# Optimization experiments

Hardware: AMD Instinct MI355X
Metric: run time of the kernel (lower is better)

The kernel has to match this reference:

```python
import jax, jax.numpy as jnp
import numpy as np
import math

D = 1024
FFN = 4096
NHEADS = 8
HEAD_DIM = D // NHEADS
RL_DIM = 4
LN_EPS = 1e-5


def _layer_norm(x, gamma, beta):
    mu = jnp.mean(x, axis=-1, keepdims=True)
    var = jnp.var(x, axis=-1, keepdims=True)
    return (x - mu) * jax.lax.rsqrt(var + LN_EPS) * gamma + beta


def setup_inputs() -> dict:
    key = jax.random.key(0)
    ks = jax.random.split(key, 12)
    B, L = 2, 2048
    s = 1.0 / math.sqrt(D)
    inp = {
        "h": jax.random.normal(ks[0], (B, L, D), dtype=jnp.float32),
        "rh": jax.random.normal(ks[1], (B, L, RL_DIM), dtype=jnp.float32),
        "Wq": jax.random.normal(ks[2], (D, D), dtype=jnp.float32) * s,
        "Wk": jax.random.normal(ks[3], (D, D), dtype=jnp.float32) * s,
        "Wv": jax.random.normal(ks[4], (D, D), dtype=jnp.float32) * s,
        "Wo": jax.random.normal(ks[5], (D, D), dtype=jnp.float32) * s,
        "Wrk": jax.random.normal(ks[6], (RL_DIM, RL_DIM), dtype=jnp.float32) * 0.5,
        "Wrq": jax.random.normal(ks[7], (RL_DIM, RL_DIM), dtype=jnp.float32) * 0.5,
        "W1": jax.random.normal(ks[8], (D, FFN), dtype=jnp.float32) * s,
        "b1": jnp.zeros((FFN,), dtype=jnp.float32),
        "W2": jax.random.normal(ks[9], (FFN, D), dtype=jnp.float32) / math.sqrt(FFN),
        "b2": jnp.zeros((D,), dtype=jnp.float32),
        "g1": jnp.ones((D,), dtype=jnp.float32),
        "be1": jnp.zeros((D,), dtype=jnp.float32),
        "g2": jnp.ones((D,), dtype=jnp.float32),
        "be2": jnp.zeros((D,), dtype=jnp.float32),
    }
    return inp


def reference(h, rh, Wq, Wk, Wv, Wo, Wrk, Wrq, W1, b1, W2, b2, g1, be1, g2, be2):
    B, L, _ = h.shape
    q = h @ Wq  # [B, L, D]
    k = h @ Wk
    v = h @ Wv
    # Faithful to the torch code: .view() reshapes (NOT transposes).
    q_ = q.reshape(B, NHEADS, L, HEAD_DIM)
    k_ = k.reshape(B, NHEADS, L, HEAD_DIM)
    v_ = v.reshape(B, NHEADS, L, HEAD_DIM)
    k_t = k_.reshape(B, NHEADS, HEAD_DIM, L)  # reshape, not transpose, as in source
    score = jnp.einsum("bnld,bndm->bnlm", q_, k_t) / math.sqrt(HEAD_DIM)
    # relative-position bias (rl=True path)
    r_k = rh @ Wrk  # [B, L, rl_dim]
    r_q = rh @ Wrq
    r_q_ = r_q[:, None]  # [B, 1, L, rl_dim]
    r_k_t = r_k[:, None].reshape(B, 1, RL_DIM, L)  # reshape, as in source
    score = score + jnp.einsum("bnlr,bnrm->bnlm", r_q_, r_k_t) / 2.0
    attn = jax.nn.softmax(score, axis=-1)
    context = jnp.einsum("bnlm,bnmd->bnld", attn, v_)
    h_sa = context.reshape(B, L, D) @ Wo
    h1 = _layer_norm(h_sa + h, g1, be1)
    hf = jax.nn.relu(h1 @ W1 + b1) @ W2 + b2
    h2 = _layer_norm(h1 + hf, g2, be2)
    return h2
```

## Files before the change

kernel.cpp:

```cpp
#include <hip/hip_runtime.h>

typedef __bf16 bf16;
typedef __bf16 bf16x8 __attribute__((ext_vector_type(8)));
typedef __bf16 bf16x4 __attribute__((ext_vector_type(4)));
typedef float  f32x4  __attribute__((ext_vector_type(4)));

#define D_     1024
#define FFN_   4096
#define NH_    8
#define HD_    128
#define L_     2048
#define B_     2
#define ROWS_  4096
#define PAIRS_ 16
#define KT_    64
#define PSTR   72
#define ALPHA_  0.08838834764831845f
#define RSCALE_ 5.656854249492381f

__device__ __forceinline__ void async16(const bf16* g, bf16* l) {
    __builtin_amdgcn_global_load_lds(
        (const __attribute__((address_space(1))) unsigned int*)g,
        (__attribute__((address_space(3))) unsigned int*)l, 16, 0, 0);
}
__device__ __forceinline__ f32x4 MFMA(bf16x8 a, bf16x8 b, f32x4 c) {
    return __builtin_amdgcn_mfma_f32_16x16x32_bf16(a, b, c, 0, 0, 0);
}

__global__ void cvt_bf16_kernel(const float* __restrict__ in, bf16* __restrict__ out) {
    long i = ((long)blockIdx.x * 256 + threadIdx.x) * 4;
    float4 v = *(const float4*)(in + i);
    bf16x4 o = {(bf16)v.x, (bf16)v.y, (bf16)v.z, (bf16)v.w};
    *(bf16x4*)(out + i) = o;
}

template<typename TI>
__global__ void transpose_to_bf16(const TI* __restrict__ in, bf16* __restrict__ out,
                                  int r, int c, long sIn, long sOut) {
    __shared__ bf16 t[32][33];
    long zi = (long)blockIdx.z * sIn;
    long zo = (long)blockIdx.z * sOut;
    int x0 = blockIdx.x * 32, y0 = blockIdx.y * 32;
    int tx = threadIdx.x & 31, ty = threadIdx.x >> 5;
#pragma unroll
    for (int i = 0; i < 4; i++)
        t[ty + i * 8][tx] = (bf16)in[zi + (long)(y0 + ty + i * 8) * c + x0 + tx];
    __syncthreads();
#pragma unroll
    for (int i = 0; i < 4; i++)
        out[zo + (long)(x0 + ty + i * 8) * r + y0 + tx] = t[tx][ty + i * 8];
}

__global__ void rqk_kernel(const float* __restrict__ rh, const float* __restrict__ Wrq,
                           const float* __restrict__ Wrk, float* __restrict__ rq,
                           float* __restrict__ rk) {
    int t = blockIdx.x * 256 + threadIdx.x;
    float4 r = *(const float4*)(rh + (long)t * 4);
    float q[4], k[4];
#pragma unroll
    for (int c = 0; c < 4; c++) {
        q[c] = r.x * Wrq[c] + r.y * Wrq[4 + c] + r.z * Wrq[8 + c] + r.w * Wrq[12 + c];
        k[c] = r.x * Wrk[c] + r.y * Wrk[4 + c] + r.z * Wrk[8 + c] + r.w * Wrk[12 + c];
    }
    float4 qo = {q[0], q[1], q[2], q[3]};
    float4 ko = {k[0], k[1], k[2], k[3]};
    *(float4*)(rq + (long)t * 4) = qo;
    *(float4*)(rk + (long)t * 4) = ko;
}

template<int BM, int EPI>
__launch_bounds__(256)
__global__ void gemm128(const bf16* __restrict__ A, const bf16* __restrict__ Bt,
                        void* __restrict__ Cv, const float* __restrict__ bias,
                        int M, int N, int K, int lda, int ldb,
                        long sA, long sB, long sC, float alpha) {
    constexpr int RF = (BM == 128) ? 4 : 2;
    __shared__ __align__(16) bf16 As[BM * 32];
    __shared__ __align__(16) bf16 Bs[128 * 32];
    const int tid  = threadIdx.x;
    const int wave = tid >> 6, lane = tid & 63;
    const int quad = lane >> 4, mr = lane & 15;
    const int bM = blockIdx.x * BM, bN = blockIdx.y * 128;
    A  += (long)blockIdx.z * sA;
    Bt += (long)blockIdx.z * sB;
    const int wr = (wave >> 1) * (BM / 2), wc = (wave & 1) * 64;

    f32x4 acc[RF][4];
#pragma unroll
    for (int r = 0; r < RF; r++)
#pragma unroll
        for (int c = 0; c < 4; c++) { f32x4 z = {0.f, 0.f, 0.f, 0.f}; acc[r][c] = z; }

    const int scol = (lane & 3) * 8;
    const bf16* Ag0; const bf16* Ag1 = nullptr;
    if (BM == 128) {
        const int srow = wave * 32 + (lane >> 2);
        Ag0 = A + (long)(bM + srow) * lda + scol;
        Ag1 = Ag0 + (long)16 * lda;
    } else {
        const int srow = wave * 16 + (lane >> 2);
        Ag0 = A + (long)(bM + srow) * lda + scol;
    }
    const int srowB = wave * 32 + (lane >> 2);
    const bf16* Bg0 = Bt + (long)(bN + srowB) * ldb + scol;
    const bf16* Bg1 = Bg0 + (long)16 * ldb;
    bf16* AsW = As + wave * (BM == 128 ? 1024 : 512);
    bf16* BsW = Bs + wave * 1024;

    for (int k0 = 0; k0 < K; k0 += 32) {
        if (BM == 128) { async16(Ag0, AsW); async16(Ag1, AsW + 512); Ag0 += 32; Ag1 += 32; }
        else           { async16(Ag0, AsW); Ag0 += 32; }
        async16(Bg0, BsW); async16(Bg1, BsW + 512);
        Bg0 += 32; Bg1 += 32;
        __syncthreads();
        bf16x8 af[RF], bfv[4];
#pragma unroll
        for (int r = 0; r < RF; r++)
            af[r] = *(const bf16x8*)(&As[(wr + r * 16 + mr) * 32 + quad * 8]);
#pragma unroll
        for (int c = 0; c < 4; c++)
            bfv[c] = *(const bf16x8*)(&Bs[(wc + c * 16 + mr) * 32 + quad * 8]);
#pragma unroll
        for (int r = 0; r < RF; r++)
#pragma unroll
            for (int c = 0; c < 4; c++)
                acc[r][c] = MFMA(af[r], bfv[c], acc[r][c]);
        __syncthreads();
    }

    const long zC = (long)blockIdx.z * sC;
    float bias_c[4];
    if (EPI & 1) {
#pragma unroll
        for (int c = 0; c < 4; c++) bias_c[c] = bias[bN + wc + c * 16 + mr];
    }
#pragma unroll
    for (int r = 0; r < RF; r++) {
#pragma unroll
        for (int c = 0; c < 4; c++) {
            const long col = bN + wc + c * 16 + mr;
#pragma unroll
            for (int i = 0; i < 4; i++) {
                const long row = bM + wr + r * 16 + quad * 4 + i;
                float v = acc[r][c][i] * alpha;
                if (EPI & 1) v += bias_c[c];
                if (EPI & 2) v = fmaxf(v, 0.f);
                if (EPI & 4) ((bf16*)Cv)[zC + row * (long)N + col] = (bf16)v;
                else         ((float*)Cv)[zC + row * (long)N + col] = v;
            }
        }
    }
}

__launch_bounds__(256, 1)
__global__ void flash_attn(const bf16* __restrict__ qb, const bf16* __restrict__ kT,
                           const bf16* __restrict__ vT, const float* __restrict__ rq,
                           const float* __restrict__ rk, bf16* __restrict__ ctx) {
    __shared__ __align__(16) bf16  Ks[2][KT_ * HD_];
    __shared__ __align__(16) bf16  Vs[2][HD_ * KT_];
    __shared__ __align__(16) float rks[2][4 * KT_];
    __shared__ __align__(16) bf16  Ps[4][32 * PSTR];

    const int tid = threadIdx.x, wave = tid >> 6, lane = tid & 63;
    const int quad = lane >> 4, mr = lane & 15;
    const int pair = blockIdx.y, b = pair >> 3;
    const int bQ = blockIdx.x * 128;
    const long PB = (long)pair * L_ * HD_;
    const bf16* Qg = qb + PB;
    const bf16* Kg = kT + PB;
    const bf16* Vg = vT + PB;
    const float* rkb = rk + (long)b * L_ * 4;

    bf16x8 Qf[2][4], Qe[2];
#pragma unroll
    for (int f = 0; f < 2; f++) {
#pragma unroll
        for (int t = 0; t < 4; t++)
            Qf[f][t] = *(const bf16x8*)(Qg + (long)(bQ + wave * 32 + f * 16 + mr) * HD_ + t * 32 + quad * 8);
        bf16x8 z = {};
        if (quad == 0) {
            float4 v = *(const float4*)(rq + ((long)b * L_ + bQ + wave * 32 + f * 16 + mr) * 4);
            z[0] = (bf16)(v.x * RSCALE_); z[1] = (bf16)(v.y * RSCALE_);
            z[2] = (bf16)(v.z * RSCALE_); z[3] = (bf16)(v.w * RSCALE_);
        }
        Qe[f] = z;
    }

    bf16x8 ones;
#pragma unroll
    for (int j = 0; j < 8; j++) ones[j] = (bf16)1.0f;

    f32x4 O[2][8], Osum[2];
#pragma unroll
    for (int f = 0; f < 2; f++) {
#pragma unroll
        for (int c = 0; c < 8; c++) { f32x4 z = {0.f, 0.f, 0.f, 0.f}; O[f][c] = z; }
        f32x4 z = {0.f, 0.f, 0.f, 0.f}; Osum[f] = z;
    }

#define STAGE_TILES(buf, kt0)                                                              \
    {                                                                                      \
        _Pragma("unroll")                                                                  \
        for (int it = 0; it < 4; it++) {                                                   \
            int G = it * 256 + tid;                                                        \
            int r1 = G >> 4, g1 = (G & 15) ^ (r1 & 15);                                    \
            async16(Kg + (long)((kt0) + r1) * HD_ + g1 * 8, &Ks[buf][(it * 256 + wave * 64) * 8]); \
            int r2 = G >> 3, g2 = (G & 7) ^ (r2 & 7);                                      \
            async16(Vg + (long)r2 * L_ + (kt0) + g2 * 8, &Vs[buf][(it * 256 + wave * 64) * 8]);    \
        }                                                                                  \
        if (tid < 64) {                                                                    \
            int r3 = tid >> 4, g3 = tid & 15;                                              \
            async16((const bf16*)(rkb + (long)r3 * L_ + (kt0) + g3 * 4), (bf16*)&rks[buf][0]); \
        }                                                                                  \
    }

    STAGE_TILES(0, 0)
    __syncthreads();

    for (int kt = 0; kt < L_ / KT_; kt++) {
        const int cur = kt & 1;
        if (kt + 1 < L_ / KT_) STAGE_TILES(cur ^ 1, (kt + 1) * KT_)

        const bf16* KsB = Ks[cur];
        const bf16* VsB = Vs[cur];
        const float* rksB = rks[cur];
        bf16* PsW = Ps[wave];

        f32x4 sc[4][2];
#pragma unroll
        for (int c = 0; c < 4; c++) {
            f32x4 s0 = {0.f, 0.f, 0.f, 0.f}, s1 = s0;
#pragma unroll
            for (int t = 0; t < 4; t++) {
                bf16x8 kf = *(const bf16x8*)(KsB + (c * 16 + mr) * HD_ + (((t * 4 + quad) ^ mr) * 8));
                s0 = MFMA(Qf[0][t], kf, s0);
                s1 = MFMA(Qf[1][t], kf, s1);
            }
            bf16x8 ke = {};
            if (quad == 0) {
                ke[0] = (bf16)rksB[0 * KT_ + c * 16 + mr];
                ke[1] = (bf16)rksB[1 * KT_ + c * 16 + mr];
                ke[2] = (bf16)rksB[2 * KT_ + c * 16 + mr];
                ke[3] = (bf16)rksB[3 * KT_ + c * 16 + mr];
            }
            s0 = MFMA(Qe[0], ke, s0);
            s1 = MFMA(Qe[1], ke, s1);
            sc[c][0] = s0; sc[c][1] = s1;
        }

#pragma unroll
        for (int f = 0; f < 2; f++) {
#pragma unroll
            for (int i = 0; i < 4; i++) {
                const int prow = (f * 16 + quad * 4 + i) * PSTR;
                PsW[prow + 0 * 16 + mr] = (bf16)__expf(sc[0][f][i] * ALPHA_);
                PsW[prow + 1 * 16 + mr] = (bf16)__expf(sc[1][f][i] * ALPHA_);
                PsW[prow + 2 * 16 + mr] = (bf16)__expf(sc[2][f][i] * ALPHA_);
                PsW[prow + 3 * 16 + mr] = (bf16)__expf(sc[3][f][i] * ALPHA_);
            }
        }

#pragma unroll
        for (int t = 0; t < 2; t++) {
            bf16x8 pf0 = *(const bf16x8*)(PsW + (0 * 16 + mr) * PSTR + t * 32 + quad * 8);
            bf16x8 pf1 = *(const bf16x8*)(PsW + (1 * 16 + mr) * PSTR + t * 32 + quad * 8);
            Osum[0] = MFMA(pf0, ones, Osum[0]);
            Osum[1] = MFMA(pf1, ones, Osum[1]);
#pragma unroll
            for (int c2 = 0; c2 < 8; c2++) {
                bf16x8 vf = *(const bf16x8*)(VsB + (c2 * 16 + mr) * KT_ + (((t * 4 + quad) ^ (mr & 7)) * 8));
                O[0][c2] = MFMA(pf0, vf, O[0][c2]);
                O[1][c2] = MFMA(pf1, vf, O[1][c2]);
            }
        }
        __syncthreads();
    }

    bf16* Cg = ctx + PB;
#pragma unroll
    for (int f = 0; f < 2; f++)
#pragma unroll
        for (int i = 0; i < 4; i++) {
            const float inv = 1.f / Osum[f][i];
            const long row = bQ + wave * 32 + f * 16 + quad * 4 + i;
#pragma unroll
            for (int c2 = 0; c2 < 8; c2++)
                Cg[row * HD_ + c2 * 16 + mr] = (bf16)(O[f][c2][i] * inv);
        }
#undef STAGE_TILES
}

__global__ void layernorm_res(const float* __restrict__ x1, const float* __restrict__ x2,
                              const float* __restrict__ g, const float* __restrict__ be,
                              float* __restrict__ outf, bf16* __restrict__ outb) {
    const int row = blockIdx.x, tid = threadIdx.x;
    const long base = (long)row * D_ + tid * 4;
    float4 a = *(const float4*)(x1 + base);
    float4 b = *(const float4*)(x2 + base);
    float x[4] = {a.x + b.x, a.y + b.y, a.z + b.z, a.w + b.w};
    float s = x[0] + x[1] + x[2] + x[3];
    float s2 = x[0] * x[0] + x[1] * x[1] + x[2] * x[2] + x[3] * x[3];
#pragma unroll
    for (int off = 32; off; off >>= 1) { s += __shfl_xor(s, off, 64); s2 += __shfl_xor(s2, off, 64); }
    __shared__ float ps[4], ps2[4];
    int wave = tid >> 6, lane = tid & 63;
    if (lane == 0) { ps[wave] = s; ps2[wave] = s2; }
    __syncthreads();
    s  = ps[0] + ps[1] + ps[2] + ps[3];
    s2 = ps2[0] + ps2[1] + ps2[2] + ps2[3];
    float mean = s * (1.f / D_);
    float var  = s2 * (1.f / D_) - mean * mean;
    float rstd = rsqrtf(var + 1e-5f);
    float4 gg = *(const float4*)(g + tid * 4);
    float4 bb = *(const float4*)(be + tid * 4);
    float y0 = (x[0] - mean) * rstd * gg.x + bb.x;
    float y1 = (x[1] - mean) * rstd * gg.y + bb.y;
    float y2 = (x[2] - mean) * rstd * gg.z + bb.z;
    float y3 = (x[3] - mean) * rstd * gg.w + bb.w;
    float4 yo = {y0, y1, y2, y3};
    *(float4*)(outf + base) = yo;
    bf16x4 ob = {(bf16)y0, (bf16)y1, (bf16)y2, (bf16)y3};
    *(bf16x4*)(outb + base) = ob;
}

template<int SK>
__global__ void layernorm_res2(const float* __restrict__ parts, const float* __restrict__ b2,
                               const float* __restrict__ x2, const float* __restrict__ g,
                               const float* __restrict__ be, float* __restrict__ outf) {
    const int row = blockIdx.x, tid = threadIdx.x;
    const long base = (long)row * D_ + tid * 4;
    float4 a = *(const float4*)(parts + base);
#pragma unroll
    for (int z = 1; z < SK; z++) {
        float4 p = *(const float4*)(parts + (long)z * ROWS_ * D_ + base);
        a.x += p.x; a.y += p.y; a.z += p.z; a.w += p.w;
    }
    float4 bb2 = *(const float4*)(b2 + tid * 4);
    float4 b = *(const float4*)(x2 + base);
    float x[4] = {a.x + bb2.x + b.x, a.y + bb2.y + b.y, a.z + bb2.z + b.z, a.w + bb2.w + b.w};
    float s = x[0] + x[1] + x[2] + x[3];
    float s2 = x[0] * x[0] + x[1] * x[1] + x[2] * x[2] + x[3] * x[3];
#pragma unroll
    for (int off = 32; off; off >>= 1) { s += __shfl_xor(s, off, 64); s2 += __shfl_xor(s2, off, 64); }
    __shared__ float ps[4], ps2[4];
    int wave = tid >> 6, lane = tid & 63;
    if (lane == 0) { ps[wave] = s; ps2[wave] = s2; }
    __syncthreads();
    s  = ps[0] + ps[1] + ps[2] + ps[3];
    s2 = ps2[0] + ps2[1] + ps2[2] + ps2[3];
    float mean = s * (1.f / D_);
    float var  = s2 * (1.f / D_) - mean * mean;
    float rstd = rsqrtf(var + 1e-5f);
    float4 gg = *(const float4*)(g + tid * 4);
    float4 bb = *(const float4*)(be + tid * 4);
    float4 yo = {(x[0] - mean) * rstd * gg.x + bb.x, (x[1] - mean) * rstd * gg.y + bb.y,
                 (x[2] - mean) * rstd * gg.z + bb.z, (x[3] - mean) * rstd * gg.w + bb.w};
    *(float4*)(outf + base) = yo;
}

extern "C" void kernel_launch(void* const* d_in, const int* in_sizes, int n_in,
                              void* d_out, int out_size, void* d_ws, size_t ws_size,
                              hipStream_t stream) {
    (void)in_sizes; (void)n_in; (void)out_size;
    const float* h   = (const float*)d_in[0];
    const float* rh  = (const float*)d_in[1];
    const float* Wq  = (const float*)d_in[2];
    const float* Wk  = (const float*)d_in[3];
    const float* Wv  = (const float*)d_in[4];
    const float* Wo  = (const float*)d_in[5];
    const float* Wrk = (const float*)d_in[6];
    const float* Wrq = (const float*)d_in[7];
    const float* W1  = (const float*)d_in[8];
    const float* b1  = (const float*)d_in[9];
    const float* W2  = (const float*)d_in[10];
    const float* b2  = (const float*)d_in[11];
    const float* g1  = (const float*)d_in[12];
    const float* be1 = (const float*)d_in[13];
    const float* g2  = (const float*)d_in[14];
    const float* be2 = (const float*)d_in[15];

    char* w = (char*)d_ws;
    size_t used = 0;
    auto alloc = [&](size_t bytes) { char* p = w + used; used += (bytes + 255) & ~(size_t)255; return p; };
    bf16*  hb   = (bf16*)alloc((size_t)ROWS_ * D_ * 2);
    bf16*  Wqt  = (bf16*)alloc((size_t)D_ * D_ * 2);
    bf16*  Wkt  = (bf16*)alloc((size_t)D_ * D_ * 2);
    bf16*  Wvt  = (bf16*)alloc((size_t)D_ * D_ * 2);
    bf16*  Wot  = (bf16*)alloc((size_t)D_ * D_ * 2);
    bf16*  W1t  = (bf16*)alloc((size_t)D_ * FFN_ * 2);
    bf16*  W2t  = (bf16*)alloc((size_t)FFN_ * D_ * 2);
    bf16*  qb   = (bf16*)alloc((size_t)ROWS_ * D_ * 2);
    bf16*  kb   = (bf16*)alloc((size_t)ROWS_ * D_ * 2);
    bf16*  vb   = (bf16*)alloc((size_t)ROWS_ * D_ * 2);
    bf16*  kT   = (bf16*)alloc((size_t)ROWS_ * D_ * 2);
    bf16*  vT   = (bf16*)alloc((size_t)ROWS_ * D_ * 2);
    float* rq   = (float*)alloc((size_t)ROWS_ * 4 * 4);
    float* rk   = (float*)alloc((size_t)ROWS_ * 4 * 4);
    float* h1   = (float*)alloc((size_t)ROWS_ * D_ * 4);
    const size_t psz = (size_t)ROWS_ * D_ * 4;
    int SK = 1;
    if (used + 4 * psz <= ws_size) SK = 4;
    else if (used + 2 * psz <= ws_size) SK = 2;
    float* P = (float*)alloc((size_t)SK * psz);
    float* hsa = P;
    bf16* ctx = hb;
    bf16* mid = qb;
    bf16* h1b = hb;

    const dim3 blk(256);
    const long BH = (long)L_ * HD_;

    cvt_bf16_kernel<<<ROWS_ * D_ / 1024, blk, 0, stream>>>(h, hb);
    transpose_to_bf16<float><<<dim3(32, 32, 1), blk, 0, stream>>>(Wq, Wqt, D_, D_, 0, 0);
    transpose_to_bf16<float><<<dim3(32, 32, 1), blk, 0, stream>>>(Wk, Wkt, D_, D_, 0, 0);
    transpose_to_bf16<float><<<dim3(32, 32, 1), blk, 0, stream>>>(Wv, Wvt, D_, D_, 0, 0);
    transpose_to_bf16<float><<<dim3(32, 32, 1), blk, 0, stream>>>(Wo, Wot, D_, D_, 0, 0);
    transpose_to_bf16<float><<<dim3(128, 32, 1), blk, 0, stream>>>(W1, W1t, D_, FFN_, 0, 0);
    transpose_to_bf16<float><<<dim3(32, 128, 1), blk, 0, stream>>>(W2, W2t, FFN_, D_, 0, 0);
    rqk_kernel<<<ROWS_ / 256, blk, 0, stream>>>(rh, Wrq, Wrk, rq, rk);
    gemm128<128, 4><<<dim3(32, 8, 3), blk, 0, stream>>>(hb, Wqt, qb, nullptr,
        ROWS_, D_, D_, D_, D_, 0, (long)D_ * D_, (long)ROWS_ * D_, 1.f);
    transpose_to_bf16<bf16><<<dim3(64, 4, PAIRS_), blk, 0, stream>>>(kb, kT, HD_, L_, BH, BH);
    transpose_to_bf16<bf16><<<dim3(4, 64, PAIRS_), blk, 0, stream>>>(vb, vT, L_, HD_, BH, BH);
    flash_attn<<<dim3(16, 16), blk, 0, stream>>>(qb, kT, vT, rq, rk, ctx);
    gemm128<64, 0><<<dim3(64, 8, 1), blk, 0, stream>>>(ctx, Wot, hsa, nullptr,
        ROWS_, D_, D_, D_, D_, 0, 0, 0, 1.f);
    layernorm_res<<<ROWS_, blk, 0, stream>>>(hsa, h, g1, be1, h1, h1b);
    gemm128<128, 7><<<dim3(32, 32, 1), blk, 0, stream>>>(h1b, W1t, mid, b1,
        ROWS_, FFN_, D_, D_, D_, 0, 0, 0, 1.f);
    {
        const int KC = FFN_ / SK;
        if (SK == 4) {
            gemm128<128, 0><<<dim3(32, 8, 4), blk, 0, stream>>>(mid, W2t, P, nullptr,
                ROWS_, D_, KC, FFN_, FFN_, KC, KC, (long)ROWS_ * D_, 1.f);
            layernorm_res2<4><<<ROWS_, blk, 0, stream>>>(P, b2, h1, g2, be2, (float*)d_out);
        } else if (SK == 2) {
            gemm128<128, 0><<<dim3(32, 8, 2), blk, 0, stream>>>(mid, W2t, P, nullptr,
                ROWS_, D_, KC, FFN_, FFN_, KC, KC, (long)ROWS_ * D_, 1.f);
            layernorm_res2<2><<<ROWS_, blk, 0, stream>>>(P, b2, h1, g2, be2, (float*)d_out);
        } else {
            gemm128<128, 0><<<dim3(32, 8, 1), blk, 0, stream>>>(mid, W2t, P, nullptr,
                ROWS_, D_, FFN_, FFN_, FFN_, 0, 0, 0, 1.f);
            layernorm_res2<1><<<ROWS_, blk, 0, stream>>>(P, b2, h1, g2, be2, (float*)d_out);
        }
    }
}
```

Measured before the change: 433.2 us.

## Split attention KV range across two blocks and add a reduction kernel

```diff
diff --git a/kernel.cpp b/kernel.cpp
--- a/kernel.cpp
+++ b/kernel.cpp
@@ -152,18 +152,21 @@
     }
 }
 
+template<int SPLIT>
 __launch_bounds__(256, 1)
 __global__ void flash_attn(const bf16* __restrict__ qb, const bf16* __restrict__ kT,
                            const bf16* __restrict__ vT, const float* __restrict__ rq,
-                           const float* __restrict__ rk, bf16* __restrict__ ctx) {
-    __shared__ __align__(16) bf16  Ks[2][KT_ * HD_];
-    __shared__ __align__(16) bf16  Vs[2][HD_ * KT_];
-    __shared__ __align__(16) float rks[2][4 * KT_];
+                           const float* __restrict__ rk, bf16* __restrict__ ctx,
+                           float* __restrict__ opart, float* __restrict__ osum) {
+    __shared__ __align__(16) bf16  Ksh[KT_ * HD_];
+    __shared__ __align__(16) bf16  Vsh[HD_ * KT_];
+    __shared__ __align__(16) float rks[4 * KT_];
     __shared__ __align__(16) bf16  Ps[4][32 * PSTR];
 
     const int tid = threadIdx.x, wave = tid >> 6, lane = tid & 63;
     const int quad = lane >> 4, mr = lane & 15;
     const int pair = blockIdx.y, b = pair >> 3;
+    const int ksp = blockIdx.z;
     const int bQ = blockIdx.x * 128;
     const long PB = (long)pair * L_ * HD_;
     const bf16* Qg = qb + PB;
@@ -190,40 +193,32 @@
 #pragma unroll
     for (int j = 0; j < 8; j++) ones[j] = (bf16)1.0f;
 
-    f32x4 O[2][8], Osum[2];
+    f32x4 O[2][8], Os[2];
 #pragma unroll
     for (int f = 0; f < 2; f++) {
 #pragma unroll
         for (int c = 0; c < 8; c++) { f32x4 z = {0.f, 0.f, 0.f, 0.f}; O[f][c] = z; }
-        f32x4 z = {0.f, 0.f, 0.f, 0.f}; Osum[f] = z;
-    }
-
-#define STAGE_TILES(buf, kt0)                                                              \
-    {                                                                                      \
-        _Pragma("unroll")                                                                  \
-        for (int it = 0; it < 4; it++) {                                                   \
-            int G = it * 256 + tid;                                                        \
-            int r1 = G >> 4, g1 = (G & 15) ^ (r1 & 15);                                    \
-            async16(Kg + (long)((kt0) + r1) * HD_ + g1 * 8, &Ks[buf][(it * 256 + wave * 64) * 8]); \
-            int r2 = G >> 3, g2 = (G & 7) ^ (r2 & 7);                                      \
-            async16(Vg + (long)r2 * L_ + (kt0) + g2 * 8, &Vs[buf][(it * 256 + wave * 64) * 8]);    \
-        }                                                                                  \
-        if (tid < 64) {                                                                    \
-            int r3 = tid >> 4, g3 = tid & 15;                                              \
-            async16((const bf16*)(rkb + (long)r3 * L_ + (kt0) + g3 * 4), (bf16*)&rks[buf][0]); \
-        }                                                                                  \
-    }
-
-    STAGE_TILES(0, 0)
-    __syncthreads();
-
-    for (int kt = 0; kt < L_ / KT_; kt++) {
-        const int cur = kt & 1;
-        if (kt + 1 < L_ / KT_) STAGE_TILES(cur ^ 1, (kt + 1) * KT_)
-
-        const bf16* KsB = Ks[cur];
-        const bf16* VsB = Vs[cur];
-        const float* rksB = rks[cur];
+        f32x4 z = {0.f, 0.f, 0.f, 0.f}; Os[f] = z;
+    }
+
+    const int tile0 = ksp * ((L_ / KT_) / SPLIT);
+    const int tile1 = tile0 + (L_ / KT_) / SPLIT;
+    for (int kt = tile0; kt < tile1; kt++) {
+        const int kt0 = kt * KT_;
+#pragma unroll
+        for (int it = 0; it < 4; it++) {
+            int G = it * 256 + tid;
+            int r1 = G >> 4, g1 = (G & 15) ^ (r1 & 15);
+            async16(Kg + (long)(kt0 + r1) * HD_ + g1 * 8, &Ksh[(it * 256 + wave * 64) * 8]);
+            int r2 = G >> 3, g2 = (G & 7) ^ (r2 & 7);
+            async16(Vg + (long)r2 * L_ + kt0 + g2 * 8, &Vsh[(it * 256 + wave * 64) * 8]);
+        }
+        if (tid < 64) {
+            int r3 = tid >> 4, g3 = tid & 15;
+            async16((const bf16*)(rkb + (long)r3 * L_ + kt0 + g3 * 4), (bf16*)&rks[0]);
+        }
+        __syncthreads();
+
         bf16* PsW = Ps[wave];
 
         f32x4 sc[4][2];
@@ -232,16 +227,16 @@
             f32x4 s0 = {0.f, 0.f, 0.f, 0.f}, s1 = s0;
 #pragma unroll
             for (int t = 0; t < 4; t++) {
-                bf16x8 kf = *(const bf16x8*)(KsB + (c * 16 + mr) * HD_ + (((t * 4 + quad) ^ mr) * 8));
+                bf16x8 kf = *(const bf16x8*)(Ksh + (c * 16 + mr) * HD_ + (((t * 4 + quad) ^ mr) * 8));
                 s0 = MFMA(Qf[0][t], kf, s0);
                 s1 = MFMA(Qf[1][t], kf, s1);
             }
             bf16x8 ke = {};
             if (quad == 0) {
-                ke[0] = (bf16)rksB[0 * KT_ + c * 16 + mr];
-                ke[1] = (bf16)rksB[1 * KT_ + c * 16 + mr];
-                ke[2] = (bf16)rksB[2 * KT_ + c * 16 + mr];
-                ke[3] = (bf16)rksB[3 * KT_ + c * 16 + mr];
+                ke[0] = (bf16)rks[0 * KT_ + c * 16 + mr];
+                ke[1] = (bf16)rks[1 * KT_ + c * 16 + mr];
+                ke[2] = (bf16)rks[2 * KT_ + c * 16 + mr];
+                ke[3] = (bf16)rks[3 * KT_ + c * 16 + mr];
             }
             s0 = MFMA(Qe[0], ke, s0);
             s1 = MFMA(Qe[1], ke, s1);
@@ -264,11 +259,11 @@
         for (int t = 0; t < 2; t++) {
             bf16x8 pf0 = *(const bf16x8*)(PsW + (0 * 16 + mr) * PSTR + t * 32 + quad * 8);
             bf16x8 pf1 = *(const bf16x8*)(PsW + (1 * 16 + mr) * PSTR + t * 32 + quad * 8);
-            Osum[0] = MFMA(pf0, ones, Osum[0]);
-            Osum[1] = MFMA(pf1, ones, Osum[1]);
+            Os[0] = MFMA(pf0, ones, Os[0]);
+            Os[1] = MFMA(pf1, ones, Os[1]);
 #pragma unroll
             for (int c2 = 0; c2 < 8; c2++) {
-                bf16x8 vf = *(const bf16x8*)(VsB + (c2 * 16 + mr) * KT_ + (((t * 4 + quad) ^ (mr & 7)) * 8));
+                bf16x8 vf = *(const bf16x8*)(Vsh + (c2 * 16 + mr) * KT_ + (((t * 4 + quad) ^ (mr & 7)) * 8));
                 O[0][c2] = MFMA(pf0, vf, O[0][c2]);
                 O[1][c2] = MFMA(pf1, vf, O[1][c2]);
             }
@@ -276,18 +271,45 @@
         __syncthreads();
     }
 
-    bf16* Cg = ctx + PB;
-#pragma unroll
-    for (int f = 0; f < 2; f++)
-#pragma unroll
-        for (int i = 0; i < 4; i++) {
-            const float inv = 1.f / Osum[f][i];
-            const long row = bQ + wave * 32 + f * 16 + quad * 4 + i;
-#pragma unroll
-            for (int c2 = 0; c2 < 8; c2++)
-                Cg[row * HD_ + c2 * 16 + mr] = (bf16)(O[f][c2][i] * inv);
-        }
-#undef STAGE_TILES
+    if (SPLIT == 1) {
+        bf16* Cg = ctx + PB;
+#pragma unroll
+        for (int f = 0; f < 2; f++)
+#pragma unroll
+            for (int i = 0; i < 4; i++) {
+                const float inv = 1.f / Os[f][i];
+                const long row = bQ + wave * 32 + f * 16 + quad * 4 + i;
+#pragma unroll
+                for (int c2 = 0; c2 < 8; c2++)
+                    Cg[row * HD_ + c2 * 16 + mr] = (bf16)(O[f][c2][i] * inv);
+            }
+    } else {
+        float* Og = opart + (long)ksp * ((long)PAIRS_ * L_ * HD_) + PB;
+        float* Sg = osum + (long)ksp * (PAIRS_ * L_) + pair * L_;
+#pragma unroll
+        for (int f = 0; f < 2; f++)
+#pragma unroll
+            for (int i = 0; i < 4; i++) {
+                const long row = bQ + wave * 32 + f * 16 + quad * 4 + i;
+#pragma unroll
+                for (int c2 = 0; c2 < 8; c2++)
+                    Og[row * HD_ + c2 * 16 + mr] = O[f][c2][i];
+                if (mr == 0) Sg[row] = Os[f][i];
+            }
+    }
+}
+
+__global__ void flash_reduce(const float* __restrict__ op, const float* __restrict__ os,
+                             bf16* __restrict__ ctx) {
+    const long PLHD = (long)PAIRS_ * L_ * HD_;
+    long e = ((long)blockIdx.x * 256 + threadIdx.x) * 4;
+    long row = e >> 7;
+    float4 a = *(const float4*)(op + e);
+    float4 b = *(const float4*)(op + PLHD + e);
+    float inv = 1.f / (os[row] + os[(long)PAIRS_ * L_ + row]);
+    bf16x4 o = {(bf16)((a.x + b.x) * inv), (bf16)((a.y + b.y) * inv),
+                (bf16)((a.z + b.z) * inv), (bf16)((a.w + b.w) * inv)};
+    *(bf16x4*)(ctx + e) = o;
 }
 
 __global__ void layernorm_res(const float* __restrict__ x1, const float* __restrict__ x2,
@@ -397,12 +419,19 @@
     float* rq   = (float*)alloc((size_t)ROWS_ * 4 * 4);
     float* rk   = (float*)alloc((size_t)ROWS_ * 4 * 4);
     float* h1   = (float*)alloc((size_t)ROWS_ * D_ * 4);
-    const size_t psz = (size_t)ROWS_ * D_ * 4;
-    int SK = 1;
-    if (used + 4 * psz <= ws_size) SK = 4;
-    else if (used + 2 * psz <= ws_size) SK = 2;
-    float* P = (float*)alloc((size_t)SK * psz);
-    float* hsa = P;
+
+    const size_t psz    = (size_t)ROWS_ * D_ * 4;
+    const size_t PLHD   = (size_t)PAIRS_ * L_ * HD_;
+    const size_t needKS = 2 * PLHD * 4 + 2 * (size_t)PAIRS_ * L_ * 4;
+    const size_t avail  = (ws_size > used) ? ws_size - used : 0;
+    const int SK = (avail >= 4 * psz) ? 4 : (avail >= 2 * psz) ? 2 : 1;
+    size_t region = (size_t)SK * psz;
+    const int KS = (avail >= (needKS > region ? needKS : region)) ? 2 : 1;
+    if (KS == 2 && needKS > region) region = needKS;
+    float* P = (float*)alloc(region);
+    float* hsa   = P;
+    float* Opart = P;
+    float* Osum  = P + 2 * PLHD;
     bf16* ctx = hb;
     bf16* mid = qb;
     bf16* h1b = hb;
@@ -422,7 +451,12 @@
         ROWS_, D_, D_, D_, D_, 0, (long)D_ * D_, (long)ROWS_ * D_, 1.f);
     transpose_to_bf16<bf16><<<dim3(64, 4, PAIRS_), blk, 0, stream>>>(kb, kT, HD_, L_, BH, BH);
     transpose_to_bf16<bf16><<<dim3(4, 64, PAIRS_), blk, 0, stream>>>(vb, vT, L_, HD_, BH, BH);
-    flash_attn<<<dim3(16, 16), blk, 0, stream>>>(qb, kT, vT, rq, rk, ctx);
+    if (KS == 2) {
+        flash_attn<2><<<dim3(16, 16, 2), blk, 0, stream>>>(qb, kT, vT, rq, rk, ctx, Opart, Osum);
+        flash_reduce<<<PAIRS_ * L_ * HD_ / 1024, blk, 0, stream>>>(Opart, Osum, ctx);
+    } else {
+        flash_attn<1><<<dim3(16, 16, 1), blk, 0, stream>>>(qb, kT, vT, rq, rk, ctx, Opart, Osum);
+    }
     gemm128<64, 0><<<dim3(64, 8, 1), blk, 0, stream>>>(ctx, Wot, hsa, nullptr,
         ROWS_, D_, D_, D_, D_, 0, 0, 0, 1.f);
     layernorm_res<<<ROWS_, blk, 0, stream>>>(hsa, h, g1, be1, h1, h1b);
```

After: 416.8 us. 3.8% less time.
